# Kernel tuning notes

Hardware: AMD Instinct MI355X
Metric: run time of the kernel (lower is better)

Reference implementation:

```python
import jax, jax.numpy as jnp
import numpy as np

IN_CH, OUT_CH = 32, 32
MODES1, MODES2 = 16, 16
B, H, W = 16, 256, 256


def setup_inputs() -> dict:
    key = jax.random.key(0)
    k1, k2, k3 = jax.random.split(key, 3)
    scale = 1.0 / (IN_CH * OUT_CH)
    x = jax.random.normal(k1, (B, IN_CH, H, W), dtype=jnp.float32)
    # weights stored as real view of complex: [..., 2] = (real, imag)
    w1 = scale * jax.random.uniform(k2, (IN_CH, OUT_CH, MODES1, MODES2, 2), dtype=jnp.float32)
    w2 = scale * jax.random.uniform(k3, (IN_CH, OUT_CH, MODES1, MODES2, 2), dtype=jnp.float32)
    return {"x": x, "w1": w1, "w2": w2}


def reference(x, w1, w2):
    m1, m2 = MODES1, MODES2
    b, _, h, w = x.shape
    x_ft = jnp.fft.rfft2(x, axes=(-2, -1))  # [B, in_ch, H, W//2+1] complex
    c1 = w1[..., 0] + 1j * w1[..., 1]       # [in_ch, out_ch, m1, m2]
    c2 = w2[..., 0] + 1j * w2[..., 1]
    o1 = jnp.einsum('bixy,ioxy->boxy', x_ft[:, :, :m1, :m2], c1)
    o2 = jnp.einsum('bixy,ioxy->boxy', x_ft[:, :, -m1:, :m2], c2)
    out_ft = jnp.zeros((b, c1.shape[1], h, w // 2 + 1), dtype=x_ft.dtype)
    out_ft = out_ft.at[:, :, :m1, :m2].set(o1)
    out_ft = out_ft.at[:, :, -m1:, :m2].set(o2)
    return jnp.fft.irfft2(out_ft, s=(h, w), axes=(-2, -1))
```

## Files before the change

### kernel.cpp

```cpp
#include <hip/hip_runtime.h>
#include <math.h>

#define BB 16
#define CC 32
#define HH 256
#define WW 256
#define NIMG (BB * CC)

typedef _Float16 f16;
typedef __attribute__((ext_vector_type(8))) _Float16 f16x8;
typedef __attribute__((ext_vector_type(4))) float f32x4;

constexpr float TWO_PI_OVER_256 = 6.28318530717958647692f / 256.0f;

#define N_TWF 8192
#define N_ACOL 32768
#define N_AINV 16384
#define N_BINV 8192

static __device__ __forceinline__ f32x4 mfma3(f16x8 ah, f16x8 al, f16x8 bh,
                                              f16x8 bl, f32x4 c) {
  c = __builtin_amdgcn_mfma_f32_16x16x32_f16(ah, bh, c, 0, 0, 0);
  c = __builtin_amdgcn_mfma_f32_16x16x32_f16(ah, bl, c, 0, 0, 0);
  c = __builtin_amdgcn_mfma_f32_16x16x32_f16(al, bh, c, 0, 0, 0);
  return c;
}

static __device__ __forceinline__ void split16(float v, f16* hi, f16* lo) {
  f16 h_ = (f16)v;
  *hi = h_;
  *lo = (f16)(v - (float)h_);
}

__global__ __launch_bounds__(256) void k_tw(f16* __restrict__ fb) {
  const int id = blockIdx.x * 256 + threadIdx.x;
  f16* twf_hi = fb;
  f16* twf_lo = twf_hi + N_TWF;
  f16* acol_hi = twf_lo + N_TWF;
  f16* acol_lo = acol_hi + N_ACOL;
  f16* ainv_hi = acol_lo + N_ACOL;
  f16* ainv_lo = ainv_hi + N_AINV;
  f16* binv_hi = ainv_lo + N_AINV;
  f16* binv_lo = binv_hi + N_BINV;

  float v;
  f16 *dh, *dl;
  if (id < N_TWF) {
    int idx = id;
    int j = idx & 7, lane = (idx >> 3) & 63, ks = (idx >> 9) & 7,
        nt = (idx >> 12) & 1;
    int col = nt * 16 + (lane & 15);
    int w = ks * 32 + ((lane >> 4) << 3) + j;
    int kx = col >> 1, ri = col & 1;
    int ph = (kx * w) & 255;
    float s, c;
    sincosf(TWO_PI_OVER_256 * (float)ph, &s, &c);
    v = ri ? -s : c;
    dh = twf_hi + idx;
    dl = twf_lo + idx;
  } else if (id < N_TWF + N_ACOL) {
    int idx = id - N_TWF;
    int j = idx & 7, lane = (idx >> 3) & 63, ks = (idx >> 9) & 7,
        mt = (idx >> 12) & 3, half = (idx >> 14) & 1;
    int row = mt * 16 + (lane & 15);
    int k = ks * 32 + ((lane >> 4) << 3) + j;
    int h = half * 128 + (k >> 1);
    int rj = k & 1;
    int zr = (row < 32) ? row : row - 32;
    int ky = (zr < 16) ? zr : 224 + zr;
    int ph = (ky * h) & 255;
    float s, c;
    sincosf(TWO_PI_OVER_256 * (float)ph, &s, &c);
    if (row < 32)
      v = rj ? s : c;
    else
      v = rj ? c : -s;
    dh = acol_hi + idx;
    dl = acol_lo + idx;
  } else if (id < N_TWF + N_ACOL + N_AINV) {
    int idx = id - N_TWF - N_ACOL;
    int j = idx & 7, lane = (idx >> 3) & 63, ks = (idx >> 9) & 1,
        mt = (idx >> 10) & 15;
    int h = mt * 16 + (lane & 15);
    int k = ks * 32 + ((lane >> 4) << 3) + j;
    int zr = k >> 1, rj = k & 1;
    int ky = (zr < 16) ? zr : 224 + zr;
    int ph = (ky * h) & 255;
    float s, c;
    sincosf(TWO_PI_OVER_256 * (float)ph, &s, &c);
    v = rj ? s : c;
    dh = ainv_hi + idx;
    dl = ainv_lo + idx;
  } else {
    int idx = id - N_TWF - N_ACOL - N_AINV;
    int j = idx & 7, lane = (idx >> 3) & 63, nt = (idx >> 9) & 15;
    int w = nt * 16 + (lane & 15);
    int k = ((lane >> 4) << 3) + j;
    int kx = k >> 1, ri = k & 1;
    int ph = (kx * w) & 255;
    float s, c;
    sincosf(TWO_PI_OVER_256 * (float)ph, &s, &c);
    float scale = ((kx == 0) ? 1.0f : 2.0f) / 65536.0f;
    v = ri ? -scale * s : scale * c;
    dh = binv_hi + idx;
    dl = binv_lo + idx;
  }
  f16 hi, lo;
  split16(v, &hi, &lo);
  *dh = hi;
  *dl = lo;
}

__global__ __launch_bounds__(256) void k_fwd(const float* __restrict__ x,
                                             const f16* __restrict__ twf_hi,
                                             const f16* __restrict__ twf_lo,
                                             const f16* __restrict__ acol_hi,
                                             const f16* __restrict__ acol_lo,
                                             float* __restrict__ Zp) {
  __shared__ __align__(16) f16 Yc_hi[16 * 260];
  __shared__ __align__(16) f16 Yc_lo[16 * 260];
  const int t = threadIdx.x, lane = t & 63, wid = t >> 6;
  const int l15 = lane & 15, kgrp = lane >> 4;
  const int img = blockIdx.x >> 1;
  const int half = blockIdx.x & 1;
  const float* xim = x + (size_t)img * (HH * WW) + half * 128 * WW;

  for (int r = 0; r < 2; ++r) {
    const int mt = r * 4 + wid;
    f32x4 acc0 = {0.f, 0.f, 0.f, 0.f}, acc1 = {0.f, 0.f, 0.f, 0.f};
    const float* ap = xim + (mt * 16 + l15) * WW + kgrp * 8;
#pragma unroll
    for (int ks = 0; ks < 8; ++ks) {
      float4 v0 = *(const float4*)(ap + ks * 32);
      float4 v1 = *(const float4*)(ap + ks * 32 + 4);
      float vv[8] = {v0.x, v0.y, v0.z, v0.w, v1.x, v1.y, v1.z, v1.w};
      f16x8 ah, al;
#pragma unroll
      for (int e = 0; e < 8; ++e) {
        f16 h_ = (f16)vv[e];
        ah[e] = h_;
        al[e] = (f16)(vv[e] - (float)h_);
      }
      const int b0 = ((0 * 8 + ks) * 64 + lane) * 8;
      const int b1 = ((1 * 8 + ks) * 64 + lane) * 8;
      f16x8 b0h = *(const f16x8*)(twf_hi + b0);
      f16x8 b0l = *(const f16x8*)(twf_lo + b0);
      f16x8 b1h = *(const f16x8*)(twf_hi + b1);
      f16x8 b1l = *(const f16x8*)(twf_lo + b1);
      acc0 = mfma3(ah, al, b0h, b0l, acc0);
      acc1 = mfma3(ah, al, b1h, b1l, acc1);
    }
#pragma unroll
    for (int nt = 0; nt < 2; ++nt) {
#pragma unroll
      for (int jj = 0; jj < 4; ++jj) {
        const int hl = mt * 16 + kgrp * 4 + jj;
        const int n = nt * 16 + l15;
        const int kx = n >> 1, ri = n & 1;
        float v = (nt == 0) ? acc0[jj] : acc1[jj];
        f16 hv = (f16)v;
        Yc_hi[kx * 260 + 2 * hl + ri] = hv;
        Yc_lo[kx * 260 + 2 * hl + ri] = (f16)(v - (float)hv);
      }
    }
  }
  __syncthreads();
  f32x4 zacc = {0.f, 0.f, 0.f, 0.f};
#pragma unroll
  for (int ks = 0; ks < 8; ++ks) {
    const int ao = ((((half * 4 + wid) * 8) + ks) * 64 + lane) * 8;
    f16x8 a_h = *(const f16x8*)(acol_hi + ao);
    f16x8 a_l = *(const f16x8*)(acol_lo + ao);
    const int bo = l15 * 260 + ks * 32 + kgrp * 8;
    f16x8 b_h = *(const f16x8*)(Yc_hi + bo);
    f16x8 b_l = *(const f16x8*)(Yc_lo + bo);
    zacc = mfma3(a_h, a_l, b_h, b_l, zacc);
  }
  float* zp = Zp + ((size_t)img * 2 + half) * 1024;
#pragma unroll
  for (int jj = 0; jj < 4; ++jj) {
    const int row = wid * 16 + kgrp * 4 + jj;
    zp[row * 16 + l15] = zacc[jj];
  }
}

__global__ __launch_bounds__(256) void k_mix(const float* __restrict__ Zp,
                                             const float* __restrict__ w1,
                                             const float* __restrict__ w2,
                                             float* __restrict__ O) {
  __shared__ float2 zs[BB][CC];
  __shared__ float2 cs[CC][CC];
  const int t = threadIdx.x;
  const int zr = blockIdx.x >> 4;
  const int kx = blockIdx.x & 15;
  const int kyi = zr & 15;
  const float* wsrc = (zr < 16) ? w1 : w2;
#pragma unroll
  for (int p = t; p < BB * CC; p += 256) {
    int b = p >> 5, i = p & 31;
    const float* zi = Zp + (size_t)(b * CC + i) * 2048;
    float re = zi[zr * 16 + kx] + zi[1024 + zr * 16 + kx];
    float im = zi[512 + zr * 16 + kx] + zi[1536 + zr * 16 + kx];
    zs[b][i] = make_float2(re, im);
  }
#pragma unroll
  for (int p = t; p < CC * CC; p += 256) {
    int i = p >> 5, oc = p & 31;
    const float* src = wsrc + ((size_t)((i * CC + oc) * 16 + kyi) * 16 + kx) * 2;
    cs[i][oc] = make_float2(src[0], src[1]);
  }
  __syncthreads();
  const int oc = t & 31;
  const int b0 = t >> 5;
#pragma unroll
  for (int pass = 0; pass < 2; ++pass) {
    const int b = b0 + pass * 8;
    float acc_r = 0.f, acc_i = 0.f;
#pragma unroll
    for (int i = 0; i < CC; ++i) {
      float2 zv = zs[b][i];
      float2 cv = cs[i][oc];
      acc_r += zv.x * cv.x - zv.y * cv.y;
      acc_i += zv.x * cv.y + zv.y * cv.x;
    }
    float2* dst = (float2*)O + (size_t)(b * CC + oc) * 512 + zr * 16 + kx;
    *dst = make_float2(acc_r, acc_i);
  }
}

__global__ __launch_bounds__(256) void k_inv(const float* __restrict__ O,
                                             const f16* __restrict__ ainv_hi,
                                             const f16* __restrict__ ainv_lo,
                                             const f16* __restrict__ binv_hi,
                                             const f16* __restrict__ binv_lo,
                                             float* __restrict__ out) {
  __shared__ float Olds[1024];
  __shared__ __align__(16) f16 Bf_hi[2048], Bf_lo[2048];
  __shared__ __align__(16) f16 T_hi[128 * 40], T_lo[128 * 40];
  const int t = threadIdx.x, lane = t & 63, wid = t >> 6;
  const int l15 = lane & 15, kgrp = lane >> 4;
  const int img = blockIdx.x >> 1;
  const int half = blockIdx.x & 1;
  {
    float4 v = ((const float4*)(O + (size_t)img * 1024))[t];
    *(float4*)&Olds[t * 4] = v;
  }
  __syncthreads();
#pragma unroll
  for (int e = 0; e < 8; ++e) {
    const int idx = e * 256 + t;
    const int nt = idx >> 10, ks = (idx >> 9) & 1, ln = (idx >> 3) & 63,
              j = idx & 7;
    const int k = ks * 32 + ((ln >> 4) << 3) + j;
    const int n = nt * 16 + (ln & 15);
    const int zr = k >> 1, rj = k & 1, kx = n >> 1, ri = n & 1;
    const float Or = Olds[(zr * 16 + kx) * 2];
    const float Oi = Olds[(zr * 16 + kx) * 2 + 1];
    const float v = (rj == 0) ? (ri == 0 ? Or : Oi) : (ri == 0 ? -Oi : Or);
    f16 hv = (f16)v;
    Bf_hi[idx] = hv;
    Bf_lo[idx] = (f16)(v - (float)hv);
  }
  __syncthreads();
#pragma unroll
  for (int mm = 0; mm < 2; ++mm) {
    const int mtl = wid * 2 + mm;
    const int mt = half * 8 + mtl;
    f32x4 acc0 = {0.f, 0.f, 0.f, 0.f}, acc1 = {0.f, 0.f, 0.f, 0.f};
#pragma unroll
    for (int ks = 0; ks < 2; ++ks) {
      const int ao = ((mt * 2 + ks) * 64 + lane) * 8;
      f16x8 a_h = *(const f16x8*)(ainv_hi + ao);
      f16x8 a_l = *(const f16x8*)(ainv_lo + ao);
      const int bo0 = ((0 * 2 + ks) * 64 + lane) * 8;
      const int bo1 = ((1 * 2 + ks) * 64 + lane) * 8;
      f16x8 b0h = *(const f16x8*)(Bf_hi + bo0);
      f16x8 b0l = *(const f16x8*)(Bf_lo + bo0);
      f16x8 b1h = *(const f16x8*)(Bf_hi + bo1);
      f16x8 b1l = *(const f16x8*)(Bf_lo + bo1);
      acc0 = mfma3(a_h, a_l, b0h, b0l, acc0);
      acc1 = mfma3(a_h, a_l, b1h, b1l, acc1);
    }
#pragma unroll
    for (int nt = 0; nt < 2; ++nt) {
#pragma unroll
      for (int jj = 0; jj < 4; ++jj) {
        const int hl = mtl * 16 + kgrp * 4 + jj;
        const int n = nt * 16 + l15;
        float v = (nt == 0) ? acc0[jj] : acc1[jj];
        f16 hv = (f16)v;
        T_hi[hl * 40 + n] = hv;
        T_lo[hl * 40 + n] = (f16)(v - (float)hv);
      }
    }
  }
  __syncthreads();
  float* op = out + (size_t)img * (HH * WW) + (size_t)half * 128 * WW;
#pragma unroll
  for (int mm = 0; mm < 2; ++mm) {
    const int mtl = wid * 2 + mm;
    const int ao = (mtl * 16 + l15) * 40 + kgrp * 8;
    f16x8 a_h = *(const f16x8*)(T_hi + ao);
    f16x8 a_l = *(const f16x8*)(T_lo + ao);
#pragma unroll 4
    for (int nt = 0; nt < 16; ++nt) {
      const int bo = (nt * 64 + lane) * 8;
      f16x8 b_h = *(const f16x8*)(binv_hi + bo);
      f16x8 b_l = *(const f16x8*)(binv_lo + bo);
      f32x4 acc = {0.f, 0.f, 0.f, 0.f};
      acc = mfma3(a_h, a_l, b_h, b_l, acc);
#pragma unroll
      for (int jj = 0; jj < 4; ++jj) {
        const int hl = mtl * 16 + kgrp * 4 + jj;
        op[(size_t)hl * WW + nt * 16 + l15] = acc[jj];
      }
    }
  }
}

extern "C" void kernel_launch(void* const* d_in, const int* in_sizes, int n_in,
                              void* d_out, int out_size, void* d_ws,
                              size_t ws_size, hipStream_t stream) {
  const float* x = (const float*)d_in[0];
  const float* w1 = (const float*)d_in[1];
  const float* w2 = (const float*)d_in[2];
  float* out = (float*)d_out;

  f16* fb = (f16*)d_ws;
  f16* twf_hi = fb;
  f16* twf_lo = twf_hi + N_TWF;
  f16* acol_hi = twf_lo + N_TWF;
  f16* acol_lo = acol_hi + N_ACOL;
  f16* ainv_hi = acol_lo + N_ACOL;
  f16* ainv_lo = ainv_hi + N_AINV;
  f16* binv_hi = ainv_lo + N_AINV;
  f16* binv_lo = binv_hi + N_BINV;
  float* Zp = (float*)(binv_lo + N_BINV);
  float* O = Zp + (size_t)NIMG * 2048;

  k_tw<<<dim3(256), dim3(256), 0, stream>>>(fb);
  k_fwd<<<dim3(NIMG * 2), dim3(256), 0, stream>>>(x, twf_hi, twf_lo, acol_hi,
                                                  acol_lo, Zp);
  k_mix<<<dim3(512), dim3(256), 0, stream>>>(Zp, w1, w2, O);
  k_inv<<<dim3(NIMG * 2), dim3(256), 0, stream>>>(O, ainv_hi, ainv_lo, binv_hi,
                                                  binv_lo, out);
}
```

Before: 88.08 us.

## Batch x loads in forward DFT and remap mix kernel for coalesced access

In the forward kernel, all sixteen float4 loads for an input row-tile are issued up front into registers before the split-f16 MFMA loop, so more memory requests are in flight at once. The spectral mix kernel is remapped so each block handles one batch and one frequency row instead of one (row, kx) pair across all batches. Zp is then read with coalesced float4 loads, and weights are read directly from global memory with kx contiguous across threads. This removes the scattered scalar gathers of Zp and weights, but weights are now re-read by each of the 16 batch blocks and the register pressure in the forward kernel grows.

```diff
diff --git a/kernel.cpp b/kernel.cpp
--- a/kernel.cpp
+++ b/kernel.cpp
@@ -129,11 +129,17 @@
     const int mt = r * 4 + wid;
     f32x4 acc0 = {0.f, 0.f, 0.f, 0.f}, acc1 = {0.f, 0.f, 0.f, 0.f};
     const float* ap = xim + (mt * 16 + l15) * WW + kgrp * 8;
+    float4 st[16];
 #pragma unroll
     for (int ks = 0; ks < 8; ++ks) {
-      float4 v0 = *(const float4*)(ap + ks * 32);
-      float4 v1 = *(const float4*)(ap + ks * 32 + 4);
-      float vv[8] = {v0.x, v0.y, v0.z, v0.w, v1.x, v1.y, v1.z, v1.w};
+      st[2 * ks] = *(const float4*)(ap + ks * 32);
+      st[2 * ks + 1] = *(const float4*)(ap + ks * 32 + 4);
+    }
+#pragma unroll
+    for (int ks = 0; ks < 8; ++ks) {
+      float vv[8] = {st[2 * ks].x,     st[2 * ks].y,     st[2 * ks].z,
+                     st[2 * ks].w,     st[2 * ks + 1].x, st[2 * ks + 1].y,
+                     st[2 * ks + 1].z, st[2 * ks + 1].w};
       f16x8 ah, al;
 #pragma unroll
       for (int e = 0; e < 8; ++e) {
@@ -188,40 +194,41 @@
                                              const float* __restrict__ w1,
                                              const float* __restrict__ w2,
                                              float* __restrict__ O) {
-  __shared__ float2 zs[BB][CC];
-  __shared__ float2 cs[CC][CC];
+  __shared__ float zsr[CC][16];
+  __shared__ float zsi[CC][16];
   const int t = threadIdx.x;
-  const int zr = blockIdx.x >> 4;
-  const int kx = blockIdx.x & 15;
+  const int b = blockIdx.x >> 5;
+  const int zr = blockIdx.x & 31;
   const int kyi = zr & 15;
   const float* wsrc = (zr < 16) ? w1 : w2;
-#pragma unroll
-  for (int p = t; p < BB * CC; p += 256) {
-    int b = p >> 5, i = p & 31;
-    const float* zi = Zp + (size_t)(b * CC + i) * 2048;
-    float re = zi[zr * 16 + kx] + zi[1024 + zr * 16 + kx];
-    float im = zi[512 + zr * 16 + kx] + zi[1536 + zr * 16 + kx];
-    zs[b][i] = make_float2(re, im);
-  }
-#pragma unroll
-  for (int p = t; p < CC * CC; p += 256) {
-    int i = p >> 5, oc = p & 31;
-    const float* src = wsrc + ((size_t)((i * CC + oc) * 16 + kyi) * 16 + kx) * 2;
-    cs[i][oc] = make_float2(src[0], src[1]);
-  }
-  __syncthreads();
-  const int oc = t & 31;
-  const int b0 = t >> 5;
+  {
+    const int i = t >> 3, reim = (t >> 2) & 1, f4 = t & 3;
+    const float* base = Zp + ((size_t)(b * CC + i) * 2) * 1024 + reim * 512 +
+                        zr * 16 + f4 * 4;
+    float4 a = *(const float4*)(base);
+    float4 c = *(const float4*)(base + 1024);
+    float4 s =
+        make_float4(a.x + c.x, a.y + c.y, a.z + c.z, a.w + c.w);
+    if (reim == 0)
+      *(float4*)&zsr[i][f4 * 4] = s;
+    else
+      *(float4*)&zsi[i][f4 * 4] = s;
+  }
+  __syncthreads();
+  const int kx = t & 15;
+  const int oc0 = t >> 4;
+  const float2* cp = (const float2*)wsrc;
 #pragma unroll
   for (int pass = 0; pass < 2; ++pass) {
-    const int b = b0 + pass * 8;
+    const int oc = oc0 + pass * 16;
     float acc_r = 0.f, acc_i = 0.f;
-#pragma unroll
+#pragma unroll 4
     for (int i = 0; i < CC; ++i) {
-      float2 zv = zs[b][i];
-      float2 cv = cs[i][oc];
-      acc_r += zv.x * cv.x - zv.y * cv.y;
-      acc_i += zv.x * cv.y + zv.y * cv.x;
+      float zre = zsr[i][kx];
+      float zim = zsi[i][kx];
+      float2 cv = cp[(size_t)(i * CC + oc) * 256 + kyi * 16 + kx];
+      acc_r += zre * cv.x - zim * cv.y;
+      acc_i += zre * cv.y + zim * cv.x;
     }
     float2* dst = (float2*)O + (size_t)(b * CC + oc) * 512 + zr * 16 + kx;
     *dst = make_float2(acc_r, acc_i);
@@ -341,7 +348,7 @@
   k_tw<<<dim3(256), dim3(256), 0, stream>>>(fb);
   k_fwd<<<dim3(NIMG * 2), dim3(256), 0, stream>>>(x, twf_hi, twf_lo, acol_hi,
                                                   acol_lo, Zp);
-  k_mix<<<dim3(512), dim3(256), 0, stream>>>(Zp, w1, w2, O);
+  k_mix<<<dim3(BB * 32), dim3(256), 0, stream>>>(Zp, w1, w2, O);
   k_inv<<<dim3(NIMG * 2), dim3(256), 0, stream>>>(O, ainv_hi, ainv_lo, binv_hi,
                                                   binv_lo, out);
 }
```

After: 78.66 us. 10.7% less time.
